# Kernel tuning notes

Hardware: AMD Instinct MI355X
Metric: run time of the kernel (lower is better)

The kernel has to match this reference:

```python
import jax, jax.numpy as jnp
import numpy as np

N_NODES = 50000
N_EDGES = 800000
HIDDEN = 128
BN_EPS = 1e-5
LEAKY_SLOPE = 0.01


def setup_inputs() -> dict:
    key = jax.random.key(0)
    ks = jax.random.split(key, 8)
    x = jax.random.normal(ks[0], (N_NODES, HIDDEN), dtype=jnp.float32)
    edge_index = jax.random.randint(ks[1], (2, N_EDGES), 0, N_NODES, dtype=jnp.int64)
    # stacked per-layer params (4 SAGEConv layers, all 128->128)
    sc = 1.0 / np.sqrt(HIDDEN)
    Wl = jax.random.normal(ks[2], (4, HIDDEN, HIDDEN), dtype=jnp.float32) * sc
    bl = jax.random.normal(ks[3], (4, HIDDEN), dtype=jnp.float32) * sc
    Wr = jax.random.normal(ks[4], (4, HIDDEN, HIDDEN), dtype=jnp.float32) * sc
    gamma = jnp.ones((4, HIDDEN), dtype=jnp.float32)
    beta = jnp.zeros((4, HIDDEN), dtype=jnp.float32)
    return {"x": x, "edge_index": edge_index, "Wl": Wl, "bl": bl,
            "Wr": Wr, "gamma": gamma, "beta": beta}


def _sage_mean_agg(x, src, dst, n):
    # gather source features per edge, scatter-mean onto destination nodes
    msg = x[src]                                                  # [E, F]
    agg = jax.ops.segment_sum(msg, dst, num_segments=n)           # [N, F]
    cnt = jax.ops.segment_sum(jnp.ones_like(dst, dtype=x.dtype), dst, num_segments=n)
    return agg / jnp.maximum(cnt, 1.0)[:, None]


def _bn_train(x, g, b):
    mu = jnp.mean(x, axis=0)
    var = jnp.mean((x - mu) ** 2, axis=0)  # biased variance (PyTorch BN normalization)
    return (x - mu) * jax.lax.rsqrt(var + BN_EPS) * g + b


def reference(x, edge_index, Wl, bl, Wr, gamma, beta):
    src, dst = edge_index[0], edge_index[1]
    n = x.shape[0]
    h = x
    for i in range(4):
        agg = _sage_mean_agg(h, src, dst, n)
        h = agg @ Wl[i] + bl[i] + h @ Wr[i]          # SAGEConv: lin_l(mean_nbr) + lin_r(root)
        h = jnp.where(h >= 0, h, LEAKY_SLOPE * h)    # leaky_relu
        h = _bn_train(h, gamma[i], beta[i])
    # dropout: eval-mode identity (deterministic reference)
    return h
```

## Files before the change

### kernel.cpp

```cpp
#include <hip/hip_runtime.h>
#include <hip/hip_bf16.h>

#define N_NODES 50000
#define N_EDGES 800000
#define F 128
#define BN_EPS 1e-5f
#define SLOPE 0.01f
#define NB 782
#define CAP 64
#define NBIN 128
#define BINSZ 391
#define QCAP2 8192
#define ABLK 512
#define AITER 7
#define PB1 6250
#define PB2 512

typedef __attribute__((ext_vector_type(8))) __bf16 bf16x8_t;
typedef __attribute__((ext_vector_type(8))) unsigned short u16x8_t;
typedef __attribute__((ext_vector_type(4))) float f32x4_t;

__device__ __forceinline__ unsigned short f2b(float f) {
    unsigned int u = __float_as_uint(f);
    unsigned int r = (u + 0x7fffu + ((u >> 16) & 1u)) >> 16;
    return (unsigned short)r;
}
__device__ __forceinline__ float b2f_lo(unsigned int v) { return __uint_as_float(v << 16); }
__device__ __forceinline__ float b2f_hi(unsigned int v) { return __uint_as_float(v & 0xffff0000u); }


__global__ __launch_bounds__(256) void bucket2_kernel(const int* __restrict__ src,
                                                      const int* __restrict__ dst,
                                                      int* __restrict__ qtail,
                                                      unsigned int* __restrict__ qdata) {
    __shared__ int counts[NBIN];
    __shared__ int cur[NBIN];
    __shared__ int base[NBIN];
    const int tid = threadIdx.x;

    for (int k = tid; k < NBIN; k += 256) { counts[k] = 0; cur[k] = 0; }
    __syncthreads();

    unsigned int pack[AITER];
    int bin[AITER];
    const int stride = ABLK * 256;
#pragma unroll
    for (int it = 0; it < AITER; ++it) {
        const int e = blockIdx.x * 256 + tid + it * stride;
        bin[it] = -1;
        if (e < N_EDGES) {
            int d = __builtin_nontemporal_load(dst + e);
            int s = __builtin_nontemporal_load(src + e);
            bin[it] = d / BINSZ;
            pack[it] = ((unsigned int)d << 16) | (unsigned int)s;
            atomicAdd(&counts[bin[it]], 1);
        }
    }
    __syncthreads();
    if (tid < NBIN) {
        int c = counts[tid];
        base[tid] = (c > 0) ? atomicAdd(&qtail[tid * 16], c) : 0;
    }
    __syncthreads();
#pragma unroll
    for (int it = 0; it < AITER; ++it) {
        if (bin[it] >= 0) {
            int slot = base[bin[it]] + atomicAdd(&cur[bin[it]], 1);
            qdata[(long)bin[it] * QCAP2 + slot] = pack[it];
        }
    }
}

__global__ __launch_bounds__(256) void scatter2_kernel(const unsigned int* __restrict__ qdata,
                                                       const int* __restrict__ qtail,
                                                       int* __restrict__ deg,
                                                       unsigned short* __restrict__ csr) {
    __shared__ int cnt[BINSZ];
    __shared__ unsigned short stage[BINSZ][CAP];
    const int b = blockIdx.x;
    const int nbase = b * BINSZ;
    const int nn = min(BINSZ, N_NODES - nbase);
    const int tid = threadIdx.x;

    for (int r = tid; r < BINSZ; r += 256) cnt[r] = 0;
    __syncthreads();

    const int n = qtail[b * 16];
    const unsigned int* q = qdata + (long)b * QCAP2;
    for (int i = tid; i < n; i += 256) {
        unsigned int p = q[i];
        int local = (int)(p >> 16) - nbase;
        int pos = atomicAdd(&cnt[local], 1);
        if (pos < CAP) stage[local][pos] = (unsigned short)(p & 0xffff);
    }
    __syncthreads();

    for (int c = tid; c < nn * (CAP / 8); c += 256) {
        const int r = c >> 3;
        const int col = (c & 7) * 8;
        *(u16x8_t*)(csr + (long)(nbase + r) * CAP + col) = *(const u16x8_t*)&stage[r][col];
    }
    for (int r = tid; r < nn; r += 256) deg[nbase + r] = min(cnt[r], CAP);
}


__global__ __launch_bounds__(256) void prep_kernel(const float* __restrict__ x,
                                                   unsigned short* __restrict__ hb,
                                                   const float* __restrict__ Wl,
                                                   const float* __restrict__ Wr,
                                                   unsigned short* __restrict__ Wt,
                                                   float* __restrict__ scale,
                                                   float* __restrict__ shift) {
    const int b = blockIdx.x;
    const int tid = threadIdx.x;
    if (b < PB1) {
        long i = (long)b * 256 + tid;
        float4 v = ((const float4*)x)[i];
        ushort4 o;
        o.x = f2b(v.x); o.y = f2b(v.y); o.z = f2b(v.z); o.w = f2b(v.w);
        ((ushort4*)hb)[i] = o;
    } else if (b < PB1 + PB2) {
        int idx = (b - PB1) * 256 + tid;
        int k = idx & 255;
        int n = (idx >> 8) & 127;
        int i = idx >> 15;
        float v = (k < F) ? Wl[((long)i * F + k) * F + n]
                          : Wr[((long)i * F + (k - F)) * F + n];
        Wt[idx] = f2b(v);
    } else {
        if (tid < F) { scale[tid] = 1.f; shift[tid] = 0.f; }
    }
}


__device__ __forceinline__ u16x8_t affine8(u16x8_t av, const float* __restrict__ sc,
                                           const float* __restrict__ sh) {
    u16x8_t r;
#pragma unroll
    for (int j = 0; j < 8; ++j) {
        float v = __uint_as_float(((unsigned int)av[j]) << 16);
        v = v * sc[j] + sh[j];
        r[j] = f2b(v);
    }
    return r;
}

#define ACC8(A, V)                               \
    A[0] += b2f_lo(V.x); A[1] += b2f_hi(V.x);    \
    A[2] += b2f_lo(V.y); A[3] += b2f_hi(V.y);    \
    A[4] += b2f_lo(V.z); A[5] += b2f_hi(V.z);    \
    A[6] += b2f_lo(V.w); A[7] += b2f_hi(V.w);

#define PACKJ(j, A) {                                                   \
    const float4 s0 = *(const float4*)(scale + q * 8 + 32 * (j));       \
    const float4 s1 = *(const float4*)(scale + q * 8 + 32 * (j) + 4);   \
    const float4 t0 = *(const float4*)(shift + q * 8 + 32 * (j));       \
    const float4 t1 = *(const float4*)(shift + q * 8 + 32 * (j) + 4);   \
    u16x8_t r;                                                          \
    r[0] = f2b(A[0] * inv * s0.x + t0.x);                               \
    r[1] = f2b(A[1] * inv * s0.y + t0.y);                               \
    r[2] = f2b(A[2] * inv * s0.z + t0.z);                               \
    r[3] = f2b(A[3] * inv * s0.w + t0.w);                               \
    r[4] = f2b(A[4] * inv * s1.x + t1.x);                               \
    r[5] = f2b(A[5] * inv * s1.y + t1.y);                               \
    r[6] = f2b(A[6] * inv * s1.z + t1.z);                               \
    r[7] = f2b(A[7] * inv * s1.w + t1.w);                               \
    areg[j] = r; }

#if __has_builtin(__builtin_amdgcn_global_load_lds)
#define STAGE_HALF(half) {                                                        \
    _Pragma("unroll")                                                             \
    for (int f = 0; f < 8; ++f) {                                                 \
        const int fid = f * 256 + tid;                                            \
        const int lf = fid & 63;                                                  \
        const int ksf = (fid >> 6) & 3;                                           \
        const int ntf = fid >> 8;                                                 \
        const int n = ntf * 16 + (lf & 15);                                       \
        const int k = (half) * 128 + ksf * 32 + (lf >> 4) * 8;                    \
        const unsigned short* gsrc = Wt + (long)n * 256 + k;                      \
        unsigned short* lbase = stage + (f * 256 + wave * 64) * 8;                \
        __builtin_amdgcn_global_load_lds(                                         \
            (const __attribute__((address_space(1))) void*)gsrc,                  \
            (__attribute__((address_space(3))) void*)lbase, 16, 0, 0);            \
    } }
#else
#define STAGE_HALF(half) {                                                        \
    _Pragma("unroll")                                                             \
    for (int f = 0; f < 8; ++f) {                                                 \
        const int fid = f * 256 + tid;                                            \
        const int lf = fid & 63;                                                  \
        const int ksf = (fid >> 6) & 3;                                           \
        const int ntf = fid >> 8;                                                 \
        const int n = ntf * 16 + (lf & 15);                                       \
        const int k = (half) * 128 + ksf * 32 + (lf >> 4) * 8;                    \
        const unsigned short* gsrc = Wt + (long)n * 256 + k;                      \
        *(u16x8_t*)(stage + fid * 8) = *(const u16x8_t*)gsrc;                     \
    } }
#endif

__global__ __launch_bounds__(256) void gemm_fused(const unsigned short* __restrict__ hin,
                                                  const int* __restrict__ deg,
                                                  const unsigned short* __restrict__ csr,
                                                  const float* __restrict__ scale,
                                                  const float* __restrict__ shift,
                                                  const unsigned short* __restrict__ Wt,
                                                  const float* __restrict__ bl,
                                                  unsigned short* __restrict__ Pb,
                                                  float* __restrict__ partial) {
    __shared__ __align__(16) char shraw[32768];
    unsigned short* stage = (unsigned short*)shraw;
    unsigned short* ep16 = (unsigned short*)shraw;
    __shared__ float lsum[4][F];
    __shared__ float lsq[4][F];

    const int tid = threadIdx.x;
    const int wave = tid >> 6, lane = tid & 63;
    const int m = lane & 15, q = lane >> 4;
    const int rbase = blockIdx.x * 64 + wave * 16;
    const int arow = rbase + m;
    const bool aval = arow < N_NODES;

    STAGE_HALF(0);

    const unsigned short* hp = hin + (long)arow * F + q * 8;
    u16x8_t hraw[4];
#pragma unroll
    for (int j = 0; j < 4; ++j) hraw[j] = (u16x8_t)0;
    if (aval) {
#pragma unroll
        for (int j = 0; j < 4; ++j) hraw[j] = *(const u16x8_t*)(hp + j * 32);
    }

    const int d = aval ? deg[arow] : 0;
    const unsigned short* crow = csr + (long)arow * CAP;
    const unsigned short* hq = hin + q * 8;
    float a0[8], a1[8], a2[8], a3[8];
#pragma unroll
    for (int j = 0; j < 8; ++j) { a0[j] = 0.f; a1[j] = 0.f; a2[j] = 0.f; a3[j] = 0.f; }

    int snext = (d > 0) ? (int)crow[0] : 0;
    for (int e = 0; e < d; ++e) {
        const int s = snext;
        if (e + 1 < d) snext = (int)crow[e + 1];
        const unsigned short* hr = hq + (long)s * F;
        uint4 v0 = *(const uint4*)(hr);
        uint4 v1 = *(const uint4*)(hr + 32);
        uint4 v2 = *(const uint4*)(hr + 64);
        uint4 v3 = *(const uint4*)(hr + 96);
        ACC8(a0, v0);
        ACC8(a1, v1);
        ACC8(a2, v2);
        ACC8(a3, v3);
    }

    u16x8_t areg[8];
#pragma unroll
    for (int j = 0; j < 8; ++j) areg[j] = (u16x8_t)0;
    if (d > 0) {
        const float inv = 1.0f / (float)d;
        PACKJ(0, a0);
        PACKJ(1, a1);
        PACKJ(2, a2);
        PACKJ(3, a3);
    }
    if (aval) {
#pragma unroll
        for (int j = 0; j < 4; ++j) {
            const int base = j * 32 + q * 8;
            areg[4 + j] = affine8(hraw[j], scale + base, shift + base);
        }
    }

    f32x4_t acc[8];
#pragma unroll
    for (int nt = 0; nt < 8; ++nt) acc[nt] = (f32x4_t){0.f, 0.f, 0.f, 0.f};

    __syncthreads();
#pragma unroll
    for (int ks = 0; ks < 4; ++ks) {
        bf16x8_t af = __builtin_bit_cast(bf16x8_t, areg[ks]);
#pragma unroll
        for (int nt = 0; nt < 8; ++nt) {
            u16x8_t bv = *(const u16x8_t*)(stage + ((nt * 4 + ks) * 64 + lane) * 8);
            bf16x8_t bf = __builtin_bit_cast(bf16x8_t, bv);
            acc[nt] = __builtin_amdgcn_mfma_f32_16x16x32_bf16(af, bf, acc[nt], 0, 0, 0);
        }
    }
    __syncthreads();
    STAGE_HALF(1);
    __syncthreads();
#pragma unroll
    for (int ks = 0; ks < 4; ++ks) {
        bf16x8_t af = __builtin_bit_cast(bf16x8_t, areg[4 + ks]);
#pragma unroll
        for (int nt = 0; nt < 8; ++nt) {
            u16x8_t bv = *(const u16x8_t*)(stage + ((nt * 4 + ks) * 64 + lane) * 8);
            bf16x8_t bf = __builtin_bit_cast(bf16x8_t, bv);
            acc[nt] = __builtin_amdgcn_mfma_f32_16x16x32_bf16(af, bf, acc[nt], 0, 0, 0);
        }
    }

    __syncthreads();

    float cs[8], cq[8];
#pragma unroll
    for (int nt = 0; nt < 8; ++nt) {
        cs[nt] = 0.f; cq[nt] = 0.f;
        const int c = nt * 16 + m;
        const float b = bl[c];
#pragma unroll
        for (int r = 0; r < 4; ++r) {
            const int rl = wave * 16 + q * 4 + r;
            float v = acc[nt][r] + b;
            v = (v >= 0.f) ? v : SLOPE * v;
            ep16[rl * 136 + c] = f2b(v);
            if (rbase + q * 4 + r < N_NODES) {
                cs[nt] += v;
                cq[nt] += v * v;
            }
        }
    }

    {
        const int rq = lane >> 4;
        const int cc = (lane & 15) * 8;
#pragma unroll
        for (int r2 = 0; r2 < 4; ++r2) {
            const int rl = wave * 16 + rq * 4 + r2;
            const int grow = blockIdx.x * 64 + rl;
            if (grow < N_NODES)
                *(u16x8_t*)(Pb + (long)grow * F + cc) = *(const u16x8_t*)(ep16 + rl * 136 + cc);
        }
    }

#pragma unroll
    for (int nt = 0; nt < 8; ++nt) {
        cs[nt] += __shfl_xor(cs[nt], 16);
        cs[nt] += __shfl_xor(cs[nt], 32);
        cq[nt] += __shfl_xor(cq[nt], 16);
        cq[nt] += __shfl_xor(cq[nt], 32);
    }
    if (lane < 16) {
#pragma unroll
        for (int nt = 0; nt < 8; ++nt) {
            lsum[wave][nt * 16 + m] = cs[nt];
            lsq[wave][nt * 16 + m] = cq[nt];
        }
    }
    __syncthreads();
    if (tid < F) {
        float s = 0.f, s2 = 0.f;
#pragma unroll
        for (int w = 0; w < 4; ++w) {
            s += lsum[w][tid];
            s2 += lsq[w][tid];
        }
        partial[(long)blockIdx.x * 256 + tid] = s;
        partial[(long)blockIdx.x * 256 + 128 + tid] = s2;
    }
}

__global__ __launch_bounds__(256) void bn_reduce(const float* __restrict__ partial,
                                                 const float* __restrict__ gamma,
                                                 const float* __restrict__ beta,
                                                 float* __restrict__ scale,
                                                 float* __restrict__ shift) {
    const int j = blockIdx.x;
    const int t = threadIdx.x;
    const int lane = t & 63, wave = t >> 6;
    float s = 0.f, s2 = 0.f;
    for (int b = t; b < NB; b += 256) {
        s += partial[(long)b * 256 + j];
        s2 += partial[(long)b * 256 + 128 + j];
    }
#pragma unroll
    for (int off = 1; off < 64; off <<= 1) {
        s += __shfl_xor(s, off);
        s2 += __shfl_xor(s2, off);
    }
    __shared__ float ls[4], lq[4];
    if (lane == 0) { ls[wave] = s; lq[wave] = s2; }
    __syncthreads();
    if (t == 0) {
        float S = ls[0] + ls[1] + ls[2] + ls[3];
        float Q = lq[0] + lq[1] + lq[2] + lq[3];
        const float inv_n = 1.0f / (float)N_NODES;
        float mu = S * inv_n;
        float var = Q * inv_n - mu * mu;
        float scl = gamma[j] * rsqrtf(var + BN_EPS);
        scale[j] = scl;
        shift[j] = beta[j] - mu * scl;
    }
}

__global__ __launch_bounds__(256) void bn_apply_f(const unsigned short* __restrict__ Pb,
                                                  float* __restrict__ out,
                                                  const float* __restrict__ scale,
                                                  const float* __restrict__ shift) {
    long i = (long)blockIdx.x * blockDim.x + threadIdx.x;
    if (i >= (long)N_NODES * (F / 8)) return;
    const int c8 = (int)(i & 15);
    uint4 v = ((const uint4*)Pb)[i];
    const float4 sc0 = ((const float4*)scale)[c8 * 2];
    const float4 sc1 = ((const float4*)scale)[c8 * 2 + 1];
    const float4 sh0 = ((const float4*)shift)[c8 * 2];
    const float4 sh1 = ((const float4*)shift)[c8 * 2 + 1];
    float4 o0, o1;
    o0.x = b2f_lo(v.x) * sc0.x + sh0.x;
    o0.y = b2f_hi(v.x) * sc0.y + sh0.y;
    o0.z = b2f_lo(v.y) * sc0.z + sh0.z;
    o0.w = b2f_hi(v.y) * sc0.w + sh0.w;
    o1.x = b2f_lo(v.z) * sc1.x + sh1.x;
    o1.y = b2f_hi(v.z) * sc1.y + sh1.y;
    o1.z = b2f_lo(v.w) * sc1.z + sh1.z;
    o1.w = b2f_hi(v.w) * sc1.w + sh1.w;
    ((float4*)out)[i * 2] = o0;
    ((float4*)out)[i * 2 + 1] = o1;
}


extern "C" void kernel_launch(void* const* d_in, const int* in_sizes, int n_in,
                              void* d_out, int out_size, void* d_ws, size_t ws_size,
                              hipStream_t stream) {
    const float* x     = (const float*)d_in[0];
    const int*   ei    = (const int*)d_in[1];
    const float* Wl    = (const float*)d_in[2];
    const float* bl    = (const float*)d_in[3];
    const float* Wr    = (const float*)d_in[4];
    const float* gamma = (const float*)d_in[5];
    const float* beta  = (const float*)d_in[6];
    float* out = (float*)d_out;

    const int* src = ei;
    const int* dst = ei + N_EDGES;

    char* w = (char*)d_ws;
    auto alloc = [&](size_t bytes) -> char* {
        char* p = w;
        w += (bytes + 255) & ~(size_t)255;
        return p;
    };
    unsigned short* hbA   = (unsigned short*)alloc((size_t)N_NODES * F * 2);
    unsigned short* hbB   = (unsigned short*)alloc((size_t)N_NODES * F * 2);
    unsigned short* Wt    = (unsigned short*)alloc((size_t)4 * F * 256 * 2);
    int*   deg      = (int*)alloc((size_t)N_NODES * 4);
    int*   qtail    = (int*)alloc((size_t)NBIN * 16 * 4);
    unsigned int* qdata = (unsigned int*)alloc((size_t)NBIN * QCAP2 * 4);
    unsigned short* csr = (unsigned short*)alloc((size_t)N_NODES * CAP * 2);
    float* partial  = (float*)alloc((size_t)NB * 256 * 4);
    float* scale    = (float*)alloc(F * 4);
    float* shift    = (float*)alloc(F * 4);

    hipMemsetAsync(qtail, 0, (size_t)NBIN * 16 * 4, stream);

    bucket2_kernel<<<ABLK, 256, 0, stream>>>(src, dst, qtail, qdata);
    scatter2_kernel<<<NBIN, 256, 0, stream>>>(qdata, qtail, deg, csr);
    prep_kernel<<<PB1 + PB2 + 1, 256, 0, stream>>>(x, hbA, Wl, Wr, Wt, scale, shift);

    const int n8 = N_NODES * (F / 8);

    unsigned short* hin = hbA;
    unsigned short* hnext = hbB;
    for (int i = 0; i < 4; ++i) {
        gemm_fused<<<NB, 256, 0, stream>>>(
            hin, deg, csr, scale, shift, Wt + (size_t)i * F * 256, bl + (size_t)i * F,
            hnext, partial);

        bn_reduce<<<F, 256, 0, stream>>>(partial, gamma + (size_t)i * F, beta + (size_t)i * F,
                                         scale, shift);

        unsigned short* t = hin; hin = hnext; hnext = t;
    }
    bn_apply_f<<<(n8 + 255) / 256, 256, 0, stream>>>(hin, out, scale, shift);
}
```

Before: 400.2 us.

## Split aggregation into slab-layout kernel with XCD-aware feature slabs

Stores bf16 node features in four column slabs of 32 features each, so each gather row is 64 bytes. Aggregation moves out of the GEMM into a separate kernel that maps block indices to slabs by XCD, so each XCD's L2 sees only one slab. It adds a zero row so padded edges read zeros without branching. In exchange it adds a kernel launch per layer and a round trip of the aggregated buffer through memory.

```diff
diff --git a/kernel.cpp b/kernel.cpp
--- a/kernel.cpp
+++ b/kernel.cpp
@@ -16,6 +16,13 @@
 #define PB1 6250
 #define PB2 512
 
+#define SLABR 50048
+#define SLABST (SLABR * 32)
+#define ZROW 50000
+#define AGG_NPB 48
+#define AGG_K 521
+#define AGG_GRID (8 * AGG_K)
+
 typedef __attribute__((ext_vector_type(8))) __bf16 bf16x8_t;
 typedef __attribute__((ext_vector_type(8))) unsigned short u16x8_t;
 typedef __attribute__((ext_vector_type(4))) float f32x4_t;
@@ -76,7 +83,7 @@
                                                        int* __restrict__ deg,
                                                        unsigned short* __restrict__ csr) {
     __shared__ int cnt[BINSZ];
-    __shared__ unsigned short stage[BINSZ][CAP];
+    __shared__ __align__(16) unsigned short stage[BINSZ][CAP];
     const int b = blockIdx.x;
     const int nbase = b * BINSZ;
     const int nn = min(BINSZ, N_NODES - nbase);
@@ -105,7 +112,8 @@
 
 
 __global__ __launch_bounds__(256) void prep_kernel(const float* __restrict__ x,
-                                                   unsigned short* __restrict__ hb,
+                                                   unsigned short* __restrict__ hbA,
+                                                   unsigned short* __restrict__ hbB,
                                                    const float* __restrict__ Wl,
                                                    const float* __restrict__ Wr,
                                                    unsigned short* __restrict__ Wt,
@@ -115,10 +123,14 @@
     const int tid = threadIdx.x;
     if (b < PB1) {
         long i = (long)b * 256 + tid;
+        const int node = (int)(i >> 5);
+        const int j = (int)(i & 31);
+        const int s = j >> 3;
+        const int cj = j & 7;
         float4 v = ((const float4*)x)[i];
         ushort4 o;
         o.x = f2b(v.x); o.y = f2b(v.y); o.z = f2b(v.z); o.w = f2b(v.w);
-        ((ushort4*)hb)[i] = o;
+        ((ushort4*)hbA)[(long)s * (SLABR * 8) + (long)node * 8 + cj] = o;
     } else if (b < PB1 + PB2) {
         int idx = (b - PB1) * 256 + tid;
         int k = idx & 255;
@@ -129,21 +141,15 @@
         Wt[idx] = f2b(v);
     } else {
         if (tid < F) { scale[tid] = 1.f; shift[tid] = 0.f; }
-    }
-}
-
-
-__device__ __forceinline__ u16x8_t affine8(u16x8_t av, const float* __restrict__ sc,
-                                           const float* __restrict__ sh) {
-    u16x8_t r;
-#pragma unroll
-    for (int j = 0; j < 8; ++j) {
-        float v = __uint_as_float(((unsigned int)av[j]) << 16);
-        v = v * sc[j] + sh[j];
-        r[j] = f2b(v);
-    }
-    return r;
-}
+        else if (tid < 160) {
+            int t = tid - 128;
+            ushort4 z; z.x = 0; z.y = 0; z.z = 0; z.w = 0;
+            ((ushort4*)hbA)[(long)(t >> 3) * (SLABR * 8) + (long)ZROW * 8 + (t & 7)] = z;
+            ((ushort4*)hbB)[(long)(t >> 3) * (SLABR * 8) + (long)ZROW * 8 + (t & 7)] = z;
+        }
+    }
+}
+
 
 #define ACC8(A, V)                               \
     A[0] += b2f_lo(V.x); A[1] += b2f_hi(V.x);    \
@@ -151,21 +157,93 @@
     A[4] += b2f_lo(V.z); A[5] += b2f_hi(V.z);    \
     A[6] += b2f_lo(V.w); A[7] += b2f_hi(V.w);
 
-#define PACKJ(j, A) {                                                   \
-    const float4 s0 = *(const float4*)(scale + q * 8 + 32 * (j));       \
-    const float4 s1 = *(const float4*)(scale + q * 8 + 32 * (j) + 4);   \
-    const float4 t0 = *(const float4*)(shift + q * 8 + 32 * (j));       \
-    const float4 t1 = *(const float4*)(shift + q * 8 + 32 * (j) + 4);   \
-    u16x8_t r;                                                          \
-    r[0] = f2b(A[0] * inv * s0.x + t0.x);                               \
-    r[1] = f2b(A[1] * inv * s0.y + t0.y);                               \
-    r[2] = f2b(A[2] * inv * s0.z + t0.z);                               \
-    r[3] = f2b(A[3] * inv * s0.w + t0.w);                               \
-    r[4] = f2b(A[4] * inv * s1.x + t1.x);                               \
-    r[5] = f2b(A[5] * inv * s1.y + t1.y);                               \
-    r[6] = f2b(A[6] * inv * s1.z + t1.z);                               \
-    r[7] = f2b(A[7] * inv * s1.w + t1.w);                               \
-    areg[j] = r; }
+__global__ __launch_bounds__(256) void agg_slab(const unsigned short* __restrict__ hb,
+                                                const int* __restrict__ deg,
+                                                const unsigned short* __restrict__ csr,
+                                                const float* __restrict__ scale,
+                                                const float* __restrict__ shift,
+                                                unsigned short* __restrict__ aggs) {
+    const int b = blockIdx.x;
+    const int xcd = b & 7;
+    const int k = b >> 3;
+    const int slab = xcd & 3;
+    const int range = k * 2 + (xcd >> 2);
+    const int tid = threadIdx.x;
+    const int wave = tid >> 6, lane = tid & 63;
+    const int n = lane >> 4;
+    const int g = (lane >> 2) & 3;
+    const int c = lane & 3;
+
+    const unsigned short* hs = hb + (long)slab * SLABST + c * 8;
+    const float4 sc0 = ((const float4*)scale)[slab * 8 + c * 2];
+    const float4 sc1 = ((const float4*)scale)[slab * 8 + c * 2 + 1];
+    const float4 sh0 = ((const float4*)shift)[slab * 8 + c * 2];
+    const float4 sh1 = ((const float4*)shift)[slab * 8 + c * 2 + 1];
+
+    const int nb = range * AGG_NPB + wave * 12;
+#pragma unroll
+    for (int qq = 0; qq < 3; ++qq) {
+        const int node = nb + qq * 4 + n;
+        const bool nval = node < N_NODES;
+        const int d = nval ? deg[node] : 0;
+        int dm = d;
+        dm = max(dm, __shfl_xor(dm, 16));
+        dm = max(dm, __shfl_xor(dm, 32));
+
+        float a[8];
+#pragma unroll
+        for (int j = 0; j < 8; ++j) a[j] = 0.f;
+
+        const int crow = node * CAP;
+        for (int w0 = 0; w0 < dm; w0 += 8) {
+            const int e0 = w0 + g;
+            const int e1 = w0 + 4 + g;
+            const int r0 = (int)csr[crow + e0];
+            const int r1 = (int)csr[crow + e1];
+            const int i0 = (e0 < d) ? r0 : ZROW;
+            const int i1 = (e1 < d) ? r1 : ZROW;
+            const uint4 v0 = *(const uint4*)(hs + (long)i0 * 32);
+            const uint4 v1 = *(const uint4*)(hs + (long)i1 * 32);
+            ACC8(a, v0);
+            ACC8(a, v1);
+        }
+#pragma unroll
+        for (int j = 0; j < 8; ++j) {
+            a[j] += __shfl_xor(a[j], 4);
+            a[j] += __shfl_xor(a[j], 8);
+        }
+        if (g == 0 && nval) {
+            u16x8_t o;
+            if (d > 0) {
+                const float inv = 1.0f / (float)d;
+                o[0] = f2b(a[0] * inv * sc0.x + sh0.x);
+                o[1] = f2b(a[1] * inv * sc0.y + sh0.y);
+                o[2] = f2b(a[2] * inv * sc0.z + sh0.z);
+                o[3] = f2b(a[3] * inv * sc0.w + sh0.w);
+                o[4] = f2b(a[4] * inv * sc1.x + sh1.x);
+                o[5] = f2b(a[5] * inv * sc1.y + sh1.y);
+                o[6] = f2b(a[6] * inv * sc1.z + sh1.z);
+                o[7] = f2b(a[7] * inv * sc1.w + sh1.w);
+            } else {
+#pragma unroll
+                for (int j = 0; j < 8; ++j) o[j] = 0;
+            }
+            *(u16x8_t*)(aggs + (long)slab * SLABST + (long)node * 32 + c * 8) = o;
+        }
+    }
+}
+
+__device__ __forceinline__ u16x8_t affine8(u16x8_t av, const float* __restrict__ sc,
+                                           const float* __restrict__ sh) {
+    u16x8_t r;
+#pragma unroll
+    for (int j = 0; j < 8; ++j) {
+        float v = __uint_as_float(((unsigned int)av[j]) << 16);
+        v = v * sc[j] + sh[j];
+        r[j] = f2b(v);
+    }
+    return r;
+}
 
 #if __has_builtin(__builtin_amdgcn_global_load_lds)
 #define STAGE_HALF(half) {                                                        \
@@ -198,15 +276,14 @@
     } }
 #endif
 
-__global__ __launch_bounds__(256) void gemm_fused(const unsigned short* __restrict__ hin,
-                                                  const int* __restrict__ deg,
-                                                  const unsigned short* __restrict__ csr,
-                                                  const float* __restrict__ scale,
-                                                  const float* __restrict__ shift,
-                                                  const unsigned short* __restrict__ Wt,
-                                                  const float* __restrict__ bl,
-                                                  unsigned short* __restrict__ Pb,
-                                                  float* __restrict__ partial) {
+__global__ __launch_bounds__(256) void gemm_mfma(const unsigned short* __restrict__ aggs,
+                                                 const unsigned short* __restrict__ hin,
+                                                 const float* __restrict__ scale,
+                                                 const float* __restrict__ shift,
+                                                 const unsigned short* __restrict__ Wt,
+                                                 const float* __restrict__ bl,
+                                                 unsigned short* __restrict__ Pb,
+                                                 float* __restrict__ partial) {
     __shared__ __align__(16) char shraw[32768];
     unsigned short* stage = (unsigned short*)shraw;
     unsigned short* ep16 = (unsigned short*)shraw;
@@ -220,54 +297,18 @@
     const int arow = rbase + m;
     const bool aval = arow < N_NODES;
 
-    STAGE_HALF(0);
-
-    const unsigned short* hp = hin + (long)arow * F + q * 8;
-    u16x8_t hraw[4];
-#pragma unroll
-    for (int j = 0; j < 4; ++j) hraw[j] = (u16x8_t)0;
+    u16x8_t areg[8];
+#pragma unroll
+    for (int j = 0; j < 8; ++j) areg[j] = (u16x8_t)0;
     if (aval) {
 #pragma unroll
-        for (int j = 0; j < 4; ++j) hraw[j] = *(const u16x8_t*)(hp + j * 32);
-    }
-
-    const int d = aval ? deg[arow] : 0;
-    const unsigned short* crow = csr + (long)arow * CAP;
-    const unsigned short* hq = hin + q * 8;
-    float a0[8], a1[8], a2[8], a3[8];
-#pragma unroll
-    for (int j = 0; j < 8; ++j) { a0[j] = 0.f; a1[j] = 0.f; a2[j] = 0.f; a3[j] = 0.f; }
-
-    int snext = (d > 0) ? (int)crow[0] : 0;
-    for (int e = 0; e < d; ++e) {
-        const int s = snext;
-        if (e + 1 < d) snext = (int)crow[e + 1];
-        const unsigned short* hr = hq + (long)s * F;
-        uint4 v0 = *(const uint4*)(hr);
-        uint4 v1 = *(const uint4*)(hr + 32);
-        uint4 v2 = *(const uint4*)(hr + 64);
-        uint4 v3 = *(const uint4*)(hr + 96);
-        ACC8(a0, v0);
-        ACC8(a1, v1);
-        ACC8(a2, v2);
-        ACC8(a3, v3);
-    }
-
-    u16x8_t areg[8];
-#pragma unroll
-    for (int j = 0; j < 8; ++j) areg[j] = (u16x8_t)0;
-    if (d > 0) {
-        const float inv = 1.0f / (float)d;
-        PACKJ(0, a0);
-        PACKJ(1, a1);
-        PACKJ(2, a2);
-        PACKJ(3, a3);
-    }
-    if (aval) {
+        for (int j = 0; j < 4; ++j)
+            areg[j] = *(const u16x8_t*)(aggs + (long)j * SLABST + (long)arow * 32 + q * 8);
 #pragma unroll
         for (int j = 0; j < 4; ++j) {
+            u16x8_t raw = *(const u16x8_t*)(hin + (long)j * SLABST + (long)arow * 32 + q * 8);
             const int base = j * 32 + q * 8;
-            areg[4 + j] = affine8(hraw[j], scale + base, shift + base);
+            areg[4 + j] = affine8(raw, scale + base, shift + base);
         }
     }
 
@@ -275,28 +316,19 @@
 #pragma unroll
     for (int nt = 0; nt < 8; ++nt) acc[nt] = (f32x4_t){0.f, 0.f, 0.f, 0.f};
 
-    __syncthreads();
-#pragma unroll
-    for (int ks = 0; ks < 4; ++ks) {
-        bf16x8_t af = __builtin_bit_cast(bf16x8_t, areg[ks]);
-#pragma unroll
-        for (int nt = 0; nt < 8; ++nt) {
-            u16x8_t bv = *(const u16x8_t*)(stage + ((nt * 4 + ks) * 64 + lane) * 8);
-            bf16x8_t bf = __builtin_bit_cast(bf16x8_t, bv);
-            acc[nt] = __builtin_amdgcn_mfma_f32_16x16x32_bf16(af, bf, acc[nt], 0, 0, 0);
-        }
-    }
-    __syncthreads();
-    STAGE_HALF(1);
-    __syncthreads();
-#pragma unroll
-    for (int ks = 0; ks < 4; ++ks) {
-        bf16x8_t af = __builtin_bit_cast(bf16x8_t, areg[4 + ks]);
-#pragma unroll
-        for (int nt = 0; nt < 8; ++nt) {
-            u16x8_t bv = *(const u16x8_t*)(stage + ((nt * 4 + ks) * 64 + lane) * 8);
-            bf16x8_t bf = __builtin_bit_cast(bf16x8_t, bv);
-            acc[nt] = __builtin_amdgcn_mfma_f32_16x16x32_bf16(af, bf, acc[nt], 0, 0, 0);
+    for (int half = 0; half < 2; ++half) {
+        if (half) __syncthreads();
+        STAGE_HALF(half);
+        __syncthreads();
+#pragma unroll
+        for (int ks = 0; ks < 4; ++ks) {
+            bf16x8_t af = __builtin_bit_cast(bf16x8_t, areg[half * 4 + ks]);
+#pragma unroll
+            for (int nt = 0; nt < 8; ++nt) {
+                u16x8_t bv = *(const u16x8_t*)(stage + ((nt * 4 + ks) * 64 + lane) * 8);
+                bf16x8_t bf = __builtin_bit_cast(bf16x8_t, bv);
+                acc[nt] = __builtin_amdgcn_mfma_f32_16x16x32_bf16(af, bf, acc[nt], 0, 0, 0);
+            }
         }
     }
 
@@ -323,13 +355,16 @@
 
     {
         const int rq = lane >> 4;
-        const int cc = (lane & 15) * 8;
+        const int ch = lane & 15;
+        const int s = ch >> 2;
+        const int cw = ch & 3;
 #pragma unroll
         for (int r2 = 0; r2 < 4; ++r2) {
             const int rl = wave * 16 + rq * 4 + r2;
             const int grow = blockIdx.x * 64 + rl;
             if (grow < N_NODES)
-                *(u16x8_t*)(Pb + (long)grow * F + cc) = *(const u16x8_t*)(ep16 + rl * 136 + cc);
+                *(u16x8_t*)(Pb + (long)s * SLABST + (long)grow * 32 + cw * 8) =
+                    *(const u16x8_t*)(ep16 + rl * 136 + ch * 8);
         }
     }
 
@@ -399,8 +434,11 @@
                                                   const float* __restrict__ shift) {
     long i = (long)blockIdx.x * blockDim.x + threadIdx.x;
     if (i >= (long)N_NODES * (F / 8)) return;
+    const int node = (int)(i >> 4);
     const int c8 = (int)(i & 15);
-    uint4 v = ((const uint4*)Pb)[i];
+    const int s = c8 >> 2;
+    const int cw = c8 & 3;
+    uint4 v = *(const uint4*)(Pb + (long)s * SLABST + (long)node * 32 + cw * 8);
     const float4 sc0 = ((const float4*)scale)[c8 * 2];
     const float4 sc1 = ((const float4*)scale)[c8 * 2 + 1];
     const float4 sh0 = ((const float4*)shift)[c8 * 2];
@@ -440,13 +478,14 @@
         w += (bytes + 255) & ~(size_t)255;
         return p;
     };
-    unsigned short* hbA   = (unsigned short*)alloc((size_t)N_NODES * F * 2);
-    unsigned short* hbB   = (unsigned short*)alloc((size_t)N_NODES * F * 2);
+    unsigned short* hbA   = (unsigned short*)alloc((size_t)4 * SLABST * 2);
+    unsigned short* hbB   = (unsigned short*)alloc((size_t)4 * SLABST * 2);
+    unsigned short* aggb  = (unsigned short*)alloc((size_t)4 * SLABST * 2);
     unsigned short* Wt    = (unsigned short*)alloc((size_t)4 * F * 256 * 2);
     int*   deg      = (int*)alloc((size_t)N_NODES * 4);
     int*   qtail    = (int*)alloc((size_t)NBIN * 16 * 4);
     unsigned int* qdata = (unsigned int*)alloc((size_t)NBIN * QCAP2 * 4);
-    unsigned short* csr = (unsigned short*)alloc((size_t)N_NODES * CAP * 2);
+    unsigned short* csr = (unsigned short*)alloc((size_t)SLABR * CAP * 2);
     float* partial  = (float*)alloc((size_t)NB * 256 * 4);
     float* scale    = (float*)alloc(F * 4);
     float* shift    = (float*)alloc(F * 4);
@@ -455,15 +494,17 @@
 
     bucket2_kernel<<<ABLK, 256, 0, stream>>>(src, dst, qtail, qdata);
     scatter2_kernel<<<NBIN, 256, 0, stream>>>(qdata, qtail, deg, csr);
-    prep_kernel<<<PB1 + PB2 + 1, 256, 0, stream>>>(x, hbA, Wl, Wr, Wt, scale, shift);
+    prep_kernel<<<PB1 + PB2 + 1, 256, 0, stream>>>(x, hbA, hbB, Wl, Wr, Wt, scale, shift);
 
     const int n8 = N_NODES * (F / 8);
 
     unsigned short* hin = hbA;
     unsigned short* hnext = hbB;
     for (int i = 0; i < 4; ++i) {
-        gemm_fused<<<NB, 256, 0, stream>>>(
-            hin, deg, csr, scale, shift, Wt + (size_t)i * F * 256, bl + (size_t)i * F,
+        agg_slab<<<AGG_GRID, 256, 0, stream>>>(hin, deg, csr, scale, shift, aggb);
+
+        gemm_mfma<<<NB, 256, 0, stream>>>(
+            aggb, hin, scale, shift, Wt + (size_t)i * F * 256, bl + (size_t)i * F,
             hnext, partial);
 
         bn_reduce<<<F, 256, 0, stream>>>(partial, gamma + (size_t)i * F, beta + (size_t)i * F,
@@ -471,5 +512,5 @@
 
         unsigned short* t = hin; hin = hnext; hnext = t;
     }
-    bn_apply_f<<<(n8 + 255) / 256, 256, 0, stream>>>(hin, out, scale, shift);
-}
+    bn_apply_f<<<(n8 + 255) / 256, 0 ? 0 : 256, 0, stream>>>(hin, out, scale, shift);
+}
```

New measurement: 352.2 us. 12.0% less time.
